# Kernel tuning notes

Measured on AMD Instinct MI355X. Metric: run time of the kernel, lower is better.

The kernel has to match this reference:

```python
import jax, jax.numpy as jnp
import numpy as np

B, C, V, P, E, H, DSC, SD = 4, 1, 64, 4, 64, 8, 256, 1024
NP = (V // P) ** 3  # 4096 patches
SCALE = 1.0 / np.sqrt(E).astype(np.float32)
LN_EPS = 1e-5


def setup_inputs() -> dict:
    key = jax.random.key(0)
    ks = jax.random.split(key, 12)
    w = lambda i, shape, s=0.02: (jax.random.normal(ks[i], shape, jnp.float32) * s)
    return {
        "vox_features": jax.random.normal(ks[0], (B, C, V, V, V), jnp.float32),
        "descriptor": jax.random.normal(ks[1], (B, SD, DSC), jnp.float32),
        "conv_w": w(2, (E, C, P, P, P), 0.1),  # Conv3d weight (OIDHW)
        "conv_b": jnp.zeros((E,), jnp.float32),
        "ln_g": jnp.ones((E,), jnp.float32),
        "ln_b": jnp.zeros((E,), jnp.float32),
        "pos_emb": jnp.zeros((1, NP, E), jnp.float32),
        "wq": w(3, (E, H * E)), "bq": jnp.zeros((H * E,), jnp.float32),
        "wk": w(4, (E, H * E)), "bk": jnp.zeros((H * E,), jnp.float32),
        "wv": w(5, (E, H * E)), "bv": jnp.zeros((H * E,), jnp.float32),
        "wd": w(6, (DSC, E)), "bd": jnp.zeros((E,), jnp.float32),
        "alpha": jnp.float32(1.0),
        "wo": w(7, (H * E, C * P ** 3)), "bo": jnp.zeros((C * P ** 3,), jnp.float32),
    }


def reference(vox_features, descriptor, conv_w, conv_b, ln_g, ln_b, pos_emb,
              wq, bq, wk, bk, wv, bv, wd, bd, alpha, wo, bo):
    # Patch embedding: Conv3d stride=kernel=P -> [B, E, V/P, V/P, V/P]
    emb = jax.lax.conv_general_dilated(
        vox_features, conv_w, window_strides=(P, P, P), padding="VALID",
        dimension_numbers=("NCDHW", "OIDHW", "NCDHW"))
    emb = emb + conv_b[None, :, None, None, None]
    emb = emb.reshape(B, E, -1).transpose(0, 2, 1)  # [B, NP, E]
    # LayerNorm over last dim (torch uses biased variance)
    mu = emb.mean(-1, keepdims=True)
    var = emb.var(-1, keepdims=True)
    emb = (emb - mu) * jax.lax.rsqrt(var + LN_EPS) * ln_g + ln_b
    vox_emb = emb + pos_emb  # [B, NP, E]

    des_emb = descriptor @ wd + bd  # [B, SD, E]

    q = (vox_emb @ wq + bq).reshape(B, NP, H, E).transpose(0, 2, 1, 3)  # [B,H,NP,E]
    k = (des_emb @ wk + bk).reshape(B, SD, H, E).transpose(0, 2, 1, 3)  # [B,H,SD,E]
    v = (des_emb @ wv + bv).reshape(B, SD, H, E).transpose(0, 2, 1, 3)  # [B,H,SD,E]

    # L2 distance: |q|^2 + |k|^2 - 2 q.k
    q2 = jnp.sum(q * q, -1, keepdims=True)                    # [B,H,NP,1]
    k2 = jnp.sum(k * k, -1)[:, :, None, :]                    # [B,H,1,SD]
    dist = q2 + k2 - 2.0 * jnp.einsum("bhqd,bhkd->bhqk", q, k)
    scores = jax.nn.softmax(alpha * jnp.exp(-dist) * SCALE, axis=-1)
    attn = jnp.einsum("bhqk,bhkd->bhqd", scores, v)
    attn = attn.transpose(0, 2, 1, 3).reshape(B, NP, H * E)
    return attn @ wo + bo  # [B, NP, C*P^3]
```

## Files before the change

kernel.cpp:

```cpp
#include <hip/hip_runtime.h>

typedef unsigned short u16;
typedef __bf16 bf16x8 __attribute__((ext_vector_type(8)));
typedef float f32x4 __attribute__((ext_vector_type(4)));

struct alignas(16) V4 { unsigned x, y, z, w; };

#if __has_builtin(__builtin_amdgcn_exp2f)
#define EXP2(x) __builtin_amdgcn_exp2f(x)
#else
#define EXP2(x) __expf((x) * 0.6931471805599453f)
#endif
#define L2E 1.4426950408889634f

__device__ __forceinline__ u16 f2b(float f) {
  unsigned u = __builtin_bit_cast(unsigned, f);
  u += 0x7FFFu + ((u >> 16) & 1u);
  return (u16)(u >> 16);
}
__device__ __forceinline__ unsigned pk2(float a, float b) {
  return (unsigned)f2b(a) | ((unsigned)f2b(b) << 16);
}
__device__ __forceinline__ unsigned pkbf(float a, float b) {
  unsigned d;
  asm("v_cvt_pk_bf16_f32 %0, %1, %2" : "=v"(d) : "v"(a), "v"(b));
  return d;
}
__device__ __forceinline__ bf16x8 asb(V4 v) { return __builtin_bit_cast(bf16x8, v); }
__device__ __forceinline__ bf16x8 mk8(unsigned a, unsigned b, unsigned c, unsigned d) {
  V4 v; v.x = a; v.y = b; v.z = c; v.w = d; return asb(v);
}
__device__ __forceinline__ V4 ldg16(const u16* p) { return *reinterpret_cast<const V4*>(p); }
__device__ __forceinline__ f32x4 mfma16(bf16x8 a, bf16x8 b, f32x4 c) {
  return __builtin_amdgcn_mfma_f32_16x16x32_bf16(a, b, c, 0, 0, 0);
}
__device__ __forceinline__ void gload_lds16(const void* g, void* l) {
  __builtin_amdgcn_global_load_lds(
      (const __attribute__((address_space(1))) int*)g,
      (__attribute__((address_space(3))) int*)l, 16, 0, 0);
}

__global__ __launch_bounds__(256) void k_prep(
    const float* __restrict__ wq, const float* __restrict__ wk,
    const float* __restrict__ wv, const float* __restrict__ wd,
    const float* __restrict__ wo, const float* __restrict__ desc,
    u16* __restrict__ wqT, u16* __restrict__ wkT, u16* __restrict__ wvT,
    u16* __restrict__ wdT, u16* __restrict__ woT, u16* __restrict__ descb) {
  int i = blockIdx.x * 256 + threadIdx.x;
  if (i < 32768) {
    int n = i >> 6, d = i & 63;
    wqT[i] = f2b(wq[d * 512 + n]);
  } else if (i < 65536) {
    int j = i - 32768; int n = j >> 6, d = j & 63;
    wkT[j] = f2b(wk[d * 512 + n]);
  } else if (i < 98304) {
    int j = i - 65536; int n = j >> 6, d = j & 63;
    wvT[j] = f2b(wv[d * 512 + n]);
  } else if (i < 114688) {
    int j = i - 98304; int e = j >> 8, v = j & 255;
    wdT[j] = f2b(wd[v * 64 + e]);
  } else if (i < 147456) {
    int j = i - 114688; int n = j >> 9, kk = j & 511;
    woT[j] = f2b(wo[kk * 64 + n]);
  } else if (i < 409600) {
    int j = (i - 147456) * 4;
    const f32x4 dv = *reinterpret_cast<const f32x4*>(desc + j);
    uint2 pw; pw.x = pk2(dv[0], dv[1]); pw.y = pk2(dv[2], dv[3]);
    *reinterpret_cast<uint2*>(descb + j) = pw;
  }
}

__global__ __launch_bounds__(256) void k_convln(
    const float* __restrict__ vox, const float* __restrict__ cw,
    const float* __restrict__ cb, const float* __restrict__ lng,
    const float* __restrict__ lnb, const float* __restrict__ pos,
    u16* __restrict__ vox_emb) {
  __shared__ float wT[64 * 65];
  __shared__ float pl[4][64];
  const int t = threadIdx.x;
  for (int i = t; i < 4096; i += 256) wT[(i & 63) * 65 + (i >> 6)] = cw[i];
  __syncthreads();
  const int w = t >> 6, lane = t & 63;
  const float cbl = cb[lane], lg = lng[lane], lb = lnb[lane];
  const int i3 = lane >> 4, j3 = (lane >> 2) & 3, k3 = lane & 3;
  for (int i = 0; i < 8; ++i) {
    const int row = blockIdx.x * 32 + w * 8 + i;
    const int b = row >> 12, np = row & 4095;
    const int pd = np >> 8, ph = (np >> 4) & 15, pw = np & 15;
    pl[w][lane] = vox[(size_t)b * 262144 + (size_t)(pd * 4 + i3) * 4096 +
                      (ph * 4 + j3) * 64 + (pw * 4 + k3)];
    float acc = cbl;
    #pragma unroll
    for (int v = 0; v < 64; ++v) acc += pl[w][v] * wT[v * 65 + lane];
    float s1 = acc, s2 = acc * acc;
    #pragma unroll
    for (int m = 1; m < 64; m <<= 1) { s1 += __shfl_xor(s1, m); s2 += __shfl_xor(s2, m); }
    const float mu = s1 * (1.0f / 64.0f);
    const float var = s2 * (1.0f / 64.0f) - mu * mu;
    const float y = (acc - mu) * rsqrtf(var + 1e-5f) * lg + lb + pos[np * 64 + lane];
    vox_emb[(size_t)row * 64 + lane] = f2b(y);
  }
}

__global__ __launch_bounds__(64) void k_des(
    const u16* __restrict__ descb, const u16* __restrict__ wdT,
    const float* __restrict__ bd, u16* __restrict__ desemb) {
  const int lane = threadIdx.x, lr = lane & 15, lc = lane >> 4;
  const int sd0 = blockIdx.x * 16, et = blockIdx.y;
  f32x4 acc = {0.f, 0.f, 0.f, 0.f};
  #pragma unroll
  for (int kc = 0; kc < 8; ++kc) {
    const bf16x8 db = asb(ldg16(descb + (size_t)(sd0 + lr) * 256 + kc * 32 + lc * 8));
    const bf16x8 wa = asb(ldg16(wdT + (size_t)(et * 16 + lr) * 256 + kc * 32 + lc * 8));
    acc = mfma16(wa, db, acc);
  }
  const f32x4 bdv = *reinterpret_cast<const f32x4*>(bd + et * 16 + lc * 4);
  uint2 pw;
  pw.x = pk2(acc[0] + bdv[0], acc[1] + bdv[1]);
  pw.y = pk2(acc[2] + bdv[2], acc[3] + bdv[3]);
  *reinterpret_cast<uint2*>(desemb + (size_t)(sd0 + lr) * 64 + et * 16 + lc * 4) = pw;
}

__global__ __launch_bounds__(64) void k_kvproj(
    const u16* __restrict__ desemb, const u16* __restrict__ wkT,
    const float* __restrict__ bk, const u16* __restrict__ wvT,
    const float* __restrict__ bv, u16* __restrict__ kb,
    float* __restrict__ ekl, u16* __restrict__ vtb) {
  const int lane = threadIdx.x, lr = lane & 15, lc = lane >> 4;
  const int x = blockIdx.x, h = blockIdx.y;
  const int b = x >> 6, sb = x & 63, sd0 = sb * 16;
  char* kbc = reinterpret_cast<char*>(kb);
  char* vtc = reinterpret_cast<char*>(vtb);
  const u16* drow = desemb + (size_t)(x * 16 + lr) * 64;
  const bf16x8 da0 = asb(ldg16(drow + lc * 8));
  const bf16x8 da1 = asb(ldg16(drow + 32 + lc * 8));
  const int sd = sd0 + lr, ktK = sd >> 6, rK = sd & 63, xrK = sd & 7;
  float sq = 0.f;
  #pragma unroll
  for (int et = 0; et < 4; ++et) {
    const int etg = h * 4 + et;
    const u16* wrow = wkT + (size_t)(etg * 16 + lr) * 64;
    f32x4 acc = {0.f, 0.f, 0.f, 0.f};
    acc = mfma16(asb(ldg16(wrow + lc * 8)), da0, acc);
    acc = mfma16(asb(ldg16(wrow + 32 + lc * 8)), da1, acc);
    const f32x4 bkv = *reinterpret_cast<const f32x4*>(bk + etg * 16 + lc * 4);
    const float k0 = acc[0] + bkv[0], k1 = acc[1] + bkv[1];
    const float k2 = acc[2] + bkv[2], k3 = acc[3] + bkv[3];
    sq += k0 * k0 + k1 * k1 + k2 * k2 + k3 * k3;
    const int col16s = (((et >> 1) * 4 + lc) ^ xrK);
    uint2 pw; pw.x = pk2(k0, k1); pw.y = pk2(k2, k3);
    *reinterpret_cast<uint2*>(kbc + (size_t)(b * 8 + h) * 131072 + ktK * 8192 +
                              rK * 128 + col16s * 16 + (et & 1) * 8) = pw;
  }
  {
    float s = sq;
    s += __shfl_xor(s, 16); s += __shfl_xor(s, 32);
    if (lc == 0) ekl[(size_t)(b * 8 + h) * 1024 + sd0 + lr] = -0.5f * s;
  }
  const int ktV = sb >> 2, kkl2 = (sb >> 1) & 1, half8 = sb & 1;
  #pragma unroll
  for (int et = 0; et < 4; ++et) {
    const int etg = h * 4 + et;
    const u16* wrow = wvT + (size_t)(etg * 16 + lr) * 64;
    f32x4 acc = {0.f, 0.f, 0.f, 0.f};
    acc = mfma16(da0, asb(ldg16(wrow + lc * 8)), acc);
    acc = mfma16(da1, asb(ldg16(wrow + 32 + lc * 8)), acc);
    const float bvs = bv[etg * 16 + lr];
    const int e = et * 16 + lr;
    const int col16s = ((kkl2 * 4 + lc) ^ (e & 7));
    uint2 pw;
    pw.x = pk2(acc[0] + bvs, acc[1] + bvs);
    pw.y = pk2(acc[2] + bvs, acc[3] + bvs);
    *reinterpret_cast<uint2*>(vtc + (size_t)(b * 8 + h) * 131072 + ktV * 8192 +
                              e * 128 + col16s * 16 + half8 * 8) = pw;
  }
}

__global__ __launch_bounds__(256, 4) void k_attn(
    const u16* __restrict__ vox_emb, const u16* __restrict__ wqT,
    const float* __restrict__ bq, const float* __restrict__ alpha,
    const u16* __restrict__ kb, const float* __restrict__ eklg,
    const u16* __restrict__ vtb, u16* __restrict__ attn) {
  __shared__ __align__(16) char Kb[2][8192];
  __shared__ __align__(16) char Vb[2][8192];
  __shared__ __align__(16) float El[2][64];
  const int t = threadIdx.x, w = t >> 6, lane = t & 63, lr = lane & 15, lc = lane >> 4;
  const int wgid = blockIdx.y * 32 + blockIdx.x;
  const int l = wgid >> 3;
  const int bh = (wgid & 7) * 4 + (l >> 5);
  const int b = bh >> 3, h = bh & 7;
  const int q0 = (l & 31) * 128 + w * 32;

  bf16x8 qf0[2], qf1[2];
  float avL[2];
  {
    bf16x8 vb0[2], vb1[2];
    #pragma unroll
    for (int g = 0; g < 2; ++g) {
      const u16* vrow = vox_emb + (size_t)(b * 4096 + q0 + g * 16 + lr) * 64;
      vb0[g] = asb(ldg16(vrow + lc * 8));
      vb1[g] = asb(ldg16(vrow + 32 + lc * 8));
    }
    float sq[2] = {0.f, 0.f};
    unsigned qd[2][4][2];
    #pragma unroll
    for (int et = 0; et < 4; ++et) {
      const u16* wrow = wqT + (size_t)((h * 4 + et) * 16 + lr) * 64;
      const bf16x8 wa0 = asb(ldg16(wrow + lc * 8));
      const bf16x8 wa1 = asb(ldg16(wrow + 32 + lc * 8));
      const f32x4 bqv = *reinterpret_cast<const f32x4*>(bq + (h * 4 + et) * 16 + lc * 4);
      #pragma unroll
      for (int g = 0; g < 2; ++g) {
        f32x4 acc = {0.f, 0.f, 0.f, 0.f};
        acc = mfma16(wa0, vb0[g], acc);
        acc = mfma16(wa1, vb1[g], acc);
        const float v0 = acc[0] + bqv[0], v1 = acc[1] + bqv[1];
        const float v2 = acc[2] + bqv[2], v3 = acc[3] + bqv[3];
        sq[g] += v0 * v0 + v1 * v1 + v2 * v2 + v3 * v3;
        qd[g][et][0] = pk2(v0, v1);
        qd[g][et][1] = pk2(v2, v3);
      }
    }
    const float ca = L2E * 0.125f * alpha[0];
    #pragma unroll
    for (int g = 0; g < 2; ++g) {
      float s = sq[g];
      s += __shfl_xor(s, 16); s += __shfl_xor(s, 32);
      avL[g] = ca * __expf(-s);
      qf0[g] = mk8(qd[g][0][0], qd[g][0][1], qd[g][1][0], qd[g][1][1]);
      qf1[g] = mk8(qd[g][2][0], qd[g][2][1], qd[g][3][0], qd[g][3][1]);
    }
  }

  const f32x4 z = {0.f, 0.f, 0.f, 0.f};
  f32x4 o[2][4];
  float dn[2] = {0.f, 0.f};
  #pragma unroll
  for (int g = 0; g < 2; ++g)
    #pragma unroll
    for (int m = 0; m < 4; ++m) o[g][m] = z;

  const char* kimg = reinterpret_cast<const char*>(kb) + (size_t)bh * 131072;
  const char* vimg = reinterpret_cast<const char*>(vtb) + (size_t)bh * 131072;
  const float* ekh = eklg + (size_t)bh * 1024;
  const int xr = lr & 7;
  const float C2 = 2.8853900817779268f;

  {
    const char* kg = kimg + w * 2048 + lane * 16;
    const char* vg = vimg + w * 2048 + lane * 16;
    gload_lds16(kg, Kb[0] + w * 2048); gload_lds16(kg + 1024, Kb[0] + w * 2048 + 1024);
    gload_lds16(vg, Vb[0] + w * 2048); gload_lds16(vg + 1024, Vb[0] + w * 2048 + 1024);
    if (w == 0 && lane < 16)
      gload_lds16(reinterpret_cast<const char*>(ekh) + lane * 16,
                  reinterpret_cast<char*>(El[0]));
  }
  __syncthreads();

  for (int tt = 0; tt < 16; ++tt) {
    const int pb = tt & 1;
    if (tt < 15) {
      const int nb = pb ^ 1;
      const char* kg = kimg + (size_t)(tt + 1) * 8192 + w * 2048 + lane * 16;
      const char* vg = vimg + (size_t)(tt + 1) * 8192 + w * 2048 + lane * 16;
      gload_lds16(kg, Kb[nb] + w * 2048); gload_lds16(kg + 1024, Kb[nb] + w * 2048 + 1024);
      gload_lds16(vg, Vb[nb] + w * 2048); gload_lds16(vg + 1024, Vb[nb] + w * 2048 + 1024);
      if (w == 0 && lane < 16)
        gload_lds16(reinterpret_cast<const char*>(ekh + (tt + 1) * 64) + lane * 16,
                    reinterpret_cast<char*>(El[nb]));
    }
    const char* Kt = Kb[pb];
    const char* Vt = Vb[pb];
    const float* Et = El[pb];
    #pragma unroll
    for (int c2 = 0; c2 < 2; ++c2) {
      const char* kr0 = Kt + (c2 * 32 + lr) * 128;
      const char* kr1 = kr0 + 2048;
      const bf16x8 ka00 = asb(*reinterpret_cast<const V4*>(kr0 + ((lc ^ xr) << 4)));
      const bf16x8 ka01 = asb(*reinterpret_cast<const V4*>(kr0 + (((lc + 4) ^ xr) << 4)));
      const bf16x8 ka10 = asb(*reinterpret_cast<const V4*>(kr1 + ((lc ^ xr) << 4)));
      const bf16x8 ka11 = asb(*reinterpret_cast<const V4*>(kr1 + (((lc + 4) ^ xr) << 4)));
      const int vcol = ((c2 * 4 + lc) ^ xr) << 4;
      const char* vrb = Vt + lr * 128 + vcol;
      const bf16x8 va0 = asb(*reinterpret_cast<const V4*>(vrb));
      const bf16x8 va1 = asb(*reinterpret_cast<const V4*>(vrb + 2048));
      const bf16x8 va2 = asb(*reinterpret_cast<const V4*>(vrb + 4096));
      const bf16x8 va3 = asb(*reinterpret_cast<const V4*>(vrb + 6144));
      const f32x4 ce0 = *reinterpret_cast<const f32x4*>(Et + c2 * 32 + lc * 4);
      const f32x4 ce1 = *reinterpret_cast<const f32x4*>(Et + c2 * 32 + 16 + lc * 4);
      #pragma unroll
      for (int g = 0; g < 2; ++g) {
        f32x4 s0 = ce0, s1 = ce1;
        s0 = mfma16(ka00, qf0[g], s0); s0 = mfma16(ka01, qf1[g], s0);
        s1 = mfma16(ka10, qf0[g], s1); s1 = mfma16(ka11, qf1[g], s1);
        const float t00 = EXP2(C2 * s0[0]), t01 = EXP2(C2 * s0[1]);
        const float t02 = EXP2(C2 * s0[2]), t03 = EXP2(C2 * s0[3]);
        const float t10 = EXP2(C2 * s1[0]), t11 = EXP2(C2 * s1[1]);
        const float t12 = EXP2(C2 * s1[2]), t13 = EXP2(C2 * s1[3]);
        const float p00 = EXP2(avL[g] * t00), p01 = EXP2(avL[g] * t01);
        const float p02 = EXP2(avL[g] * t02), p03 = EXP2(avL[g] * t03);
        const float p10 = EXP2(avL[g] * t10), p11 = EXP2(avL[g] * t11);
        const float p12 = EXP2(avL[g] * t12), p13 = EXP2(avL[g] * t13);
        dn[g] += ((p00 + p01) + (p02 + p03)) + ((p10 + p11) + (p12 + p13));
        const bf16x8 pf = mk8(pkbf(p00, p01), pkbf(p02, p03),
                              pkbf(p10, p11), pkbf(p12, p13));
        o[g][0] = mfma16(va0, pf, o[g][0]);
        o[g][1] = mfma16(va1, pf, o[g][1]);
        o[g][2] = mfma16(va2, pf, o[g][2]);
        o[g][3] = mfma16(va3, pf, o[g][3]);
      }
    }
    __syncthreads();
  }

  u16* obase = attn + (size_t)(b * 4096 + q0 + lr) * 512 + h * 64 + lc * 4;
  #pragma unroll
  for (int g = 0; g < 2; ++g) {
    float s = dn[g];
    s += __shfl_xor(s, 16); s += __shfl_xor(s, 32);
    const float inv = 1.0f / s;
    #pragma unroll
    for (int m = 0; m < 4; ++m) {
      uint2 pw;
      pw.x = pk2(o[g][m][0] * inv, o[g][m][1] * inv);
      pw.y = pk2(o[g][m][2] * inv, o[g][m][3] * inv);
      *reinterpret_cast<uint2*>(obase + (size_t)g * 16 * 512 + m * 16) = pw;
    }
  }
}

__global__ __launch_bounds__(64) void k_out(
    const u16* __restrict__ attn, const u16* __restrict__ woT,
    const float* __restrict__ bo, float* __restrict__ out) {
  const int lane = threadIdx.x, lr = lane & 15, lc = lane >> 4;
  const int np0 = blockIdx.x * 16;
  const u16* arow = attn + (size_t)(np0 + lr) * 512;
  f32x4 acc[4] = {{0.f,0.f,0.f,0.f},{0.f,0.f,0.f,0.f},{0.f,0.f,0.f,0.f},{0.f,0.f,0.f,0.f}};
  #pragma unroll
  for (int kc = 0; kc < 16; ++kc) {
    const bf16x8 bfr = asb(ldg16(arow + kc * 32 + lc * 8));
    #pragma unroll
    for (int et = 0; et < 4; ++et) {
      const bf16x8 wa = asb(ldg16(woT + (size_t)(et * 16 + lr) * 512 + kc * 32 + lc * 8));
      acc[et] = mfma16(wa, bfr, acc[et]);
    }
  }
  #pragma unroll
  for (int et = 0; et < 4; ++et) {
    const f32x4 bov = *reinterpret_cast<const f32x4*>(bo + et * 16 + lc * 4);
    const f32x4 r = acc[et] + bov;
    *reinterpret_cast<f32x4*>(out + (size_t)(np0 + lr) * 64 + et * 16 + lc * 4) = r;
  }
}

extern "C" void kernel_launch(void* const* d_in, const int* in_sizes, int n_in,
                              void* d_out, int out_size, void* d_ws, size_t ws_size,
                              hipStream_t stream) {
  (void)in_sizes; (void)n_in; (void)out_size; (void)ws_size;
  const float* vox   = (const float*)d_in[0];
  const float* desc  = (const float*)d_in[1];
  const float* cw    = (const float*)d_in[2];
  const float* cb    = (const float*)d_in[3];
  const float* lng   = (const float*)d_in[4];
  const float* lnb   = (const float*)d_in[5];
  const float* pos   = (const float*)d_in[6];
  const float* wq    = (const float*)d_in[7];
  const float* bq    = (const float*)d_in[8];
  const float* wk    = (const float*)d_in[9];
  const float* bk    = (const float*)d_in[10];
  const float* wv    = (const float*)d_in[11];
  const float* bv    = (const float*)d_in[12];
  const float* wd    = (const float*)d_in[13];
  const float* bd    = (const float*)d_in[14];
  const float* alpha = (const float*)d_in[15];
  const float* wo    = (const float*)d_in[16];
  const float* bo    = (const float*)d_in[17];
  float* out = (float*)d_out;

  char* ws = (char*)d_ws;
  size_t off = 0;
  auto alloc = [&](size_t bytes) {
    char* p = ws + off;
    off += (bytes + 255) & ~(size_t)255;
    return p;
  };
  u16*   vox_emb = (u16*)alloc((size_t)16384 * 64 * 2);
  u16*   descb   = (u16*)alloc((size_t)4096 * 256 * 2);
  u16*   desemb  = (u16*)alloc((size_t)4096 * 64 * 2);
  u16*   kb      = (u16*)alloc((size_t)4096 * 512 * 2);
  u16*   vtb     = (u16*)alloc((size_t)4096 * 512 * 2);
  float* ekl     = (float*)alloc((size_t)32768 * 4);
  u16*   attn    = (u16*)alloc((size_t)16384 * 512 * 2);
  u16*   wqT     = (u16*)alloc((size_t)32768 * 2);
  u16*   wkT     = (u16*)alloc((size_t)32768 * 2);
  u16*   wvT     = (u16*)alloc((size_t)32768 * 2);
  u16*   wdT     = (u16*)alloc((size_t)16384 * 2);
  u16*   woT     = (u16*)alloc((size_t)32768 * 2);

  k_prep<<<1600, 256, 0, stream>>>(wq, wk, wv, wd, wo, desc, wqT, wkT, wvT, wdT, woT, descb);
  k_convln<<<512, 256, 0, stream>>>(vox, cw, cb, lng, lnb, pos, vox_emb);
  k_des<<<dim3(256, 4), 64, 0, stream>>>(descb, wdT, bd, desemb);
  k_kvproj<<<dim3(256, 8), 64, 0, stream>>>(desemb, wkT, bk, wvT, bv, kb, ekl, vtb);
  k_attn<<<dim3(32, 32), 256, 0, stream>>>(vox_emb, wqT, bq, alpha, kb, ekl, vtb, attn);
  k_out<<<1024, 64, 0, stream>>>(attn, woT, bo, out);
}
```

Measured before the change: 97.08 us.

## Merge prep with conv-LN launch and fold descriptor projection into KV projection

The weight/descriptor conversion kernel and the conv+LayerNorm kernel become one launch, with block ranges dispatching to each role. The descriptor projection kernel is folded into the K/V projection kernel: each block recomputes its 16x64 des_emb tile through MFMA into shared memory, so the intermediate buffer and its global round trip go away. This cuts two kernel launches. In exchange, des_emb is recomputed redundantly for each of the 8 heads, and the prep blocks share a launch with conv blocks that carry the larger shared-memory footprint.

New measurement: 103.1 us. 1.06x slower.

```diff
diff --git a/kernel.cpp b/kernel.cpp
--- a/kernel.cpp
+++ b/kernel.cpp
@@ -40,51 +40,52 @@
       (__attribute__((address_space(3))) int*)l, 16, 0, 0);
 }
 
-__global__ __launch_bounds__(256) void k_prep(
+__global__ __launch_bounds__(256) void k_pre(
     const float* __restrict__ wq, const float* __restrict__ wk,
     const float* __restrict__ wv, const float* __restrict__ wd,
     const float* __restrict__ wo, const float* __restrict__ desc,
-    u16* __restrict__ wqT, u16* __restrict__ wkT, u16* __restrict__ wvT,
-    u16* __restrict__ wdT, u16* __restrict__ woT, u16* __restrict__ descb) {
-  int i = blockIdx.x * 256 + threadIdx.x;
-  if (i < 32768) {
-    int n = i >> 6, d = i & 63;
-    wqT[i] = f2b(wq[d * 512 + n]);
-  } else if (i < 65536) {
-    int j = i - 32768; int n = j >> 6, d = j & 63;
-    wkT[j] = f2b(wk[d * 512 + n]);
-  } else if (i < 98304) {
-    int j = i - 65536; int n = j >> 6, d = j & 63;
-    wvT[j] = f2b(wv[d * 512 + n]);
-  } else if (i < 114688) {
-    int j = i - 98304; int e = j >> 8, v = j & 255;
-    wdT[j] = f2b(wd[v * 64 + e]);
-  } else if (i < 147456) {
-    int j = i - 114688; int n = j >> 9, kk = j & 511;
-    woT[j] = f2b(wo[kk * 64 + n]);
-  } else if (i < 409600) {
-    int j = (i - 147456) * 4;
-    const f32x4 dv = *reinterpret_cast<const f32x4*>(desc + j);
-    uint2 pw; pw.x = pk2(dv[0], dv[1]); pw.y = pk2(dv[2], dv[3]);
-    *reinterpret_cast<uint2*>(descb + j) = pw;
-  }
-}
-
-__global__ __launch_bounds__(256) void k_convln(
     const float* __restrict__ vox, const float* __restrict__ cw,
     const float* __restrict__ cb, const float* __restrict__ lng,
     const float* __restrict__ lnb, const float* __restrict__ pos,
+    u16* __restrict__ wqT, u16* __restrict__ wkT, u16* __restrict__ wvT,
+    u16* __restrict__ wdT, u16* __restrict__ woT, u16* __restrict__ descb,
     u16* __restrict__ vox_emb) {
   __shared__ float wT[64 * 65];
   __shared__ float pl[4][64];
   const int t = threadIdx.x;
+  if (blockIdx.x < 1600) {
+    int i = blockIdx.x * 256 + t;
+    if (i < 32768) {
+      int n = i >> 6, d = i & 63;
+      wqT[i] = f2b(wq[d * 512 + n]);
+    } else if (i < 65536) {
+      int j = i - 32768; int n = j >> 6, d = j & 63;
+      wkT[j] = f2b(wk[d * 512 + n]);
+    } else if (i < 98304) {
+      int j = i - 65536; int n = j >> 6, d = j & 63;
+      wvT[j] = f2b(wv[d * 512 + n]);
+    } else if (i < 114688) {
+      int j = i - 98304; int e = j >> 8, v = j & 255;
+      wdT[j] = f2b(wd[v * 64 + e]);
+    } else if (i < 147456) {
+      int j = i - 114688; int n = j >> 9, kk = j & 511;
+      woT[j] = f2b(wo[kk * 64 + n]);
+    } else if (i < 409600) {
+      int j = (i - 147456) * 4;
+      const f32x4 dv = *reinterpret_cast<const f32x4*>(desc + j);
+      uint2 pw; pw.x = pk2(dv[0], dv[1]); pw.y = pk2(dv[2], dv[3]);
+      *reinterpret_cast<uint2*>(descb + j) = pw;
+    }
+    return;
+  }
+  const int bx = blockIdx.x - 1600;
   for (int i = t; i < 4096; i += 256) wT[(i & 63) * 65 + (i >> 6)] = cw[i];
   __syncthreads();
   const int w = t >> 6, lane = t & 63;
   const float cbl = cb[lane], lg = lng[lane], lb = lnb[lane];
   const int i3 = lane >> 4, j3 = (lane >> 2) & 3, k3 = lane & 3;
   for (int i = 0; i < 8; ++i) {
-    const int row = blockIdx.x * 32 + w * 8 + i;
+    const int row = bx * 32 + w * 8 + i;
     const int b = row >> 12, np = row & 4095;
     const int pd = np >> 8, ph = (np >> 4) & 15, pw = np & 15;
     pl[w][lane] = vox[(size_t)b * 262144 + (size_t)(pd * 4 + i3) * 4096 +
@@ -102,38 +103,44 @@
   }
 }
 
-__global__ __launch_bounds__(64) void k_des(
+__global__ __launch_bounds__(64) void k_kvproj(
     const u16* __restrict__ descb, const u16* __restrict__ wdT,
-    const float* __restrict__ bd, u16* __restrict__ desemb) {
-  const int lane = threadIdx.x, lr = lane & 15, lc = lane >> 4;
-  const int sd0 = blockIdx.x * 16, et = blockIdx.y;
-  f32x4 acc = {0.f, 0.f, 0.f, 0.f};
-  #pragma unroll
-  for (int kc = 0; kc < 8; ++kc) {
-    const bf16x8 db = asb(ldg16(descb + (size_t)(sd0 + lr) * 256 + kc * 32 + lc * 8));
-    const bf16x8 wa = asb(ldg16(wdT + (size_t)(et * 16 + lr) * 256 + kc * 32 + lc * 8));
-    acc = mfma16(wa, db, acc);
-  }
-  const f32x4 bdv = *reinterpret_cast<const f32x4*>(bd + et * 16 + lc * 4);
-  uint2 pw;
-  pw.x = pk2(acc[0] + bdv[0], acc[1] + bdv[1]);
-  pw.y = pk2(acc[2] + bdv[2], acc[3] + bdv[3]);
-  *reinterpret_cast<uint2*>(desemb + (size_t)(sd0 + lr) * 64 + et * 16 + lc * 4) = pw;
-}
-
-__global__ __launch_bounds__(64) void k_kvproj(
-    const u16* __restrict__ desemb, const u16* __restrict__ wkT,
+    const float* __restrict__ bd, const u16* __restrict__ wkT,
     const float* __restrict__ bk, const u16* __restrict__ wvT,
     const float* __restrict__ bv, u16* __restrict__ kb,
     float* __restrict__ ekl, u16* __restrict__ vtb) {
+  __shared__ u16 dl[16 * 72];
   const int lane = threadIdx.x, lr = lane & 15, lc = lane >> 4;
   const int x = blockIdx.x, h = blockIdx.y;
   const int b = x >> 6, sb = x & 63, sd0 = sb * 16;
   char* kbc = reinterpret_cast<char*>(kb);
   char* vtc = reinterpret_cast<char*>(vtb);
-  const u16* drow = desemb + (size_t)(x * 16 + lr) * 64;
-  const bf16x8 da0 = asb(ldg16(drow + lc * 8));
-  const bf16x8 da1 = asb(ldg16(drow + 32 + lc * 8));
+
+  {
+    bf16x8 db[8];
+    #pragma unroll
+    for (int kc = 0; kc < 8; ++kc)
+      db[kc] = asb(ldg16(descb + (size_t)(x * 16 + lr) * 256 + kc * 32 + lc * 8));
+    #pragma unroll
+    for (int et = 0; et < 4; ++et) {
+      f32x4 acc = {0.f, 0.f, 0.f, 0.f};
+      #pragma unroll
+      for (int kc = 0; kc < 8; ++kc) {
+        const bf16x8 wa = asb(ldg16(wdT + (size_t)(et * 16 + lr) * 256 + kc * 32 + lc * 8));
+        acc = mfma16(wa, db[kc], acc);
+      }
+      const f32x4 bdv = *reinterpret_cast<const f32x4*>(bd + et * 16 + lc * 4);
+      uint2 pw;
+      pw.x = pk2(acc[0] + bdv[0], acc[1] + bdv[1]);
+      pw.y = pk2(acc[2] + bdv[2], acc[3] + bdv[3]);
+      *reinterpret_cast<uint2*>(dl + lr * 72 + et * 16 + lc * 4) = pw;
+    }
+  }
+  __syncthreads();
+  const u16* drow = dl + lr * 72;
+  const bf16x8 da0 = asb(*reinterpret_cast<const V4*>(drow + lc * 8));
+  const bf16x8 da1 = asb(*reinterpret_cast<const V4*>(drow + 32 + lc * 8));
+
   const int sd = sd0 + lr, ktK = sd >> 6, rK = sd & 63, xrK = sd & 7;
   float sq = 0.f;
   #pragma unroll
@@ -386,7 +393,6 @@
   };
   u16*   vox_emb = (u16*)alloc((size_t)16384 * 64 * 2);
   u16*   descb   = (u16*)alloc((size_t)4096 * 256 * 2);
-  u16*   desemb  = (u16*)alloc((size_t)4096 * 64 * 2);
   u16*   kb      = (u16*)alloc((size_t)4096 * 512 * 2);
   u16*   vtb     = (u16*)alloc((size_t)4096 * 512 * 2);
   float* ekl     = (float*)alloc((size_t)32768 * 4);
@@ -397,10 +403,10 @@
   u16*   wdT     = (u16*)alloc((size_t)16384 * 2);
   u16*   woT     = (u16*)alloc((size_t)32768 * 2);
 
-  k_prep<<<1600, 256, 0, stream>>>(wq, wk, wv, wd, wo, desc, wqT, wkT, wvT, wdT, woT, descb);
-  k_convln<<<512, 256, 0, stream>>>(vox, cw, cb, lng, lnb, pos, vox_emb);
-  k_des<<<dim3(256, 4), 64, 0, stream>>>(descb, wdT, bd, desemb);
-  k_kvproj<<<dim3(256, 8), 64, 0, stream>>>(desemb, wkT, bk, wvT, bv, kb, ekl, vtb);
+  k_pre<<<2112, 256, 0, stream>>>(wq, wk, wv, wd, wo, desc, vox, cw, cb, lng, lnb,
+                                  pos, wqT, wkT, wvT, wdT, woT, descb, vox_emb);
+  k_kvproj<<<dim3(256, 8), 64, 0, stream>>>(descb, wdT, bd, wkT, bk, wvT, bv,
+                                            kb, ekl, vtb);
   k_attn<<<dim3(32, 32), 256, 0, stream>>>(vox_emb, wqT, bq, alpha, kb, ekl, vtb, attn);
   k_out<<<1024, 64, 0, stream>>>(attn, woT, bo, out);
 }
```
